# Kernel optimization log

Hardware: AMD Instinct MI355X
Metric: run time of the kernel (lower is better)

## Reference

```python
import jax, jax.numpy as jnp
import numpy as np

D_IN = 2048
D_OUT = 2048
H = 16
QK_ROPE = 64
QK_NOPE = 64
QK_HEAD = QK_NOPE + QK_ROPE  # 128
V_HEAD = 128
KV_RANK = 512
THETA = 10000.0
EPS = 1e-6


def rms_norm(x, w):
    var = jnp.mean(x * x, axis=-1, keepdims=True)
    return x * jax.lax.rsqrt(var + EPS) * w


def apply_rope(x, theta=THETA):
    # x: [B, S, H, D] with D even; interleaved-pair rotation (torchtune style)
    B, S, NH, D = x.shape
    half = D // 2
    freqs = 1.0 / (theta ** (jnp.arange(0, D, 2, dtype=jnp.float32) / D))  # [D/2]
    ang = jnp.arange(S, dtype=jnp.float32)[:, None] * freqs[None, :]       # [S, D/2]
    cos = jnp.cos(ang)[None, :, None, :]  # [1,S,1,D/2]
    sin = jnp.sin(ang)[None, :, None, :]
    xp = x.reshape(B, S, NH, half, 2)
    x1, x2 = xp[..., 0], xp[..., 1]
    out = jnp.stack([x1 * cos - x2 * sin, x2 * cos + x1 * sin], axis=-1)
    return out.reshape(B, S, NH, D).astype(x.dtype)


def setup_inputs() -> dict:
    key = jax.random.key(0)
    ks = jax.random.split(key, 6)
    B, S = 2, 2048
    s = lambda fan_in: 1.0 / np.sqrt(fan_in)
    x = jax.random.normal(ks[0], (B, S, D_IN), dtype=jnp.float32)
    w_query = jax.random.uniform(ks[1], (D_IN, H * QK_HEAD), jnp.float32, -s(D_IN), s(D_IN))
    wkv_a = jax.random.uniform(ks[2], (D_IN, KV_RANK + QK_ROPE), jnp.float32, -s(D_IN), s(D_IN))
    wkv_b = jax.random.uniform(ks[3], (KV_RANK, H * (QK_NOPE + V_HEAD)), jnp.float32, -s(KV_RANK), s(KV_RANK))
    kv_norm_w = jnp.ones((KV_RANK,), jnp.float32)
    out_proj_w = jax.random.uniform(ks[4], (H * V_HEAD, D_OUT), jnp.float32, -s(H * V_HEAD), s(H * V_HEAD))
    return {"x": x, "w_query": w_query, "wkv_a": wkv_a, "wkv_b": wkv_b,
            "kv_norm_w": kv_norm_w, "out_proj_w": out_proj_w}


def reference(x, w_query, wkv_a, wkv_b, kv_norm_w, out_proj_w):
    B, S, _ = x.shape
    scale = QK_HEAD ** -0.5
    # queries (no q-lora)
    q = (x @ w_query).reshape(B, S, H, QK_HEAD)
    # low-rank KV compression
    kv = x @ wkv_a                                    # [B,S,KV_RANK+QK_ROPE]
    kv_c, k_pe = kv[..., :KV_RANK], kv[..., KV_RANK:]
    kv_dec = (rms_norm(kv_c, kv_norm_w) @ wkv_b).reshape(B, S, H, QK_NOPE + V_HEAD)
    k_nope, v = kv_dec[..., :QK_NOPE], kv_dec[..., QK_NOPE:]
    k_pe = jnp.broadcast_to(k_pe[:, :, None, :], (B, S, H, QK_ROPE))
    q_nope, q_pe = q[..., :QK_NOPE], q[..., QK_NOPE:]
    q_pe = apply_rope(q_pe)
    k_pe = apply_rope(k_pe)
    queries = jnp.concatenate([q_nope, q_pe], axis=-1)   # [B,S,H,QK_HEAD]
    keys = jnp.concatenate([k_nope, k_pe], axis=-1)
    # attention
    scores = jnp.einsum('bqhd,bkhd->bhqk', queries, keys) * scale
    mask = jnp.triu(jnp.ones((S, S), dtype=bool), k=1)
    scores = jnp.where(mask[None, None], -jnp.inf, scores)
    attn = jax.nn.softmax(scores.astype(jnp.float32), axis=-1).astype(x.dtype)
    out = jnp.einsum('bhqk,bkhd->bqhd', attn, v).reshape(B, S, H * V_HEAD)
    return out @ out_proj_w
```

## Files before the change

kernel.cpp:

```cpp
#include <hip/hip_runtime.h>
#include <hip/hip_bf16.h>
#include <math.h>

#define BATCH   2
#define SEQ     2048
#define D_IN    2048
#define NHEAD   16
#define QK_ROPE 64
#define QK_NOPE 64
#define QK_HEAD 128
#define V_HEAD  128
#define KV_RANK 512
#define KV_W    640
#define NTOK    (BATCH*SEQ)
#define EPS_F   1e-6f

typedef unsigned short u16;
typedef short bf16x8 __attribute__((ext_vector_type(8)));
typedef float f32x4  __attribute__((ext_vector_type(4)));

__device__ __forceinline__ u16 f2bf(float f) {
    unsigned u = __float_as_uint(f);
    return (u16)((u + 0x7fffu + ((u >> 16) & 1u)) >> 16);
}
__device__ __forceinline__ float bf2f(u16 u) {
    return __uint_as_float(((unsigned)u) << 16);
}
__device__ __forceinline__ float exp2_hw(float x) {
    float r;
    asm volatile("v_exp_f32 %0, %1\n\ts_nop 0" : "=v"(r) : "v"(x));
    return r;
}
__device__ __forceinline__ void gload16(const void* g, void* l) {
    __builtin_amdgcn_global_load_lds((const __attribute__((address_space(1))) unsigned int*)g,
                                     (__attribute__((address_space(3))) unsigned int*)l, 16, 0, 0);
}

__global__ __launch_bounds__(256) void convert_bf16(const float* __restrict__ src,
                                                    u16* __restrict__ dst, int n4) {
    int gid = blockIdx.x * 256 + threadIdx.x;
    if (gid >= n4) return;
    float4 v = ((const float4*)src)[gid];
    unsigned lo = (unsigned)f2bf(v.x) | ((unsigned)f2bf(v.y) << 16);
    unsigned hi = (unsigned)f2bf(v.z) | ((unsigned)f2bf(v.w) << 16);
    ((uint2*)dst)[gid] = make_uint2(lo, hi);
}

__global__ __launch_bounds__(256) void transpose_bf16(const float* __restrict__ src,
                                                      u16* __restrict__ dst,
                                                      int N, int K) {
    __shared__ float tile[32][33];
    const int nb = blockIdx.x * 32, kb = blockIdx.y * 32;
    const int tx = threadIdx.x, ty = threadIdx.y;
#pragma unroll
    for (int i = 0; i < 4; ++i) {
        int k = kb + ty + 8 * i, n = nb + tx;
        tile[ty + 8 * i][tx] = (n < N) ? src[(size_t)k * N + n] : 0.f;
    }
    __syncthreads();
#pragma unroll
    for (int i = 0; i < 4; ++i) {
        int n = nb + ty + 8 * i, k = kb + tx;
        dst[(size_t)n * K + k] = f2bf(tile[tx][ty + 8 * i]);
    }
}

__global__ __launch_bounds__(256) void rope_table_kernel(float* __restrict__ tab) {
    int gid = blockIdx.x * 256 + threadIdx.x;
    int i = gid & 31, s = gid >> 5;
    float freq = __expf(-(float)(2 * i) / 64.0f * 9.210340371976184f);
    float ang = (float)s * freq;
    tab[2 * gid]     = cosf(ang);
    tab[2 * gid + 1] = sinf(ang);
}

template <int EPI>
__global__ __launch_bounds__(256) void gemm_core(const u16* __restrict__ A,
                                                 const u16* __restrict__ BT,
                                                 void* __restrict__ out0,
                                                 void* __restrict__ out1,
                                                 const float* __restrict__ tab,
                                                 int M, int N, int K, float oscale) {
    __shared__ u16 As[128 * 32];
    __shared__ u16 Bs[128 * 32];
    const int tid = threadIdx.x;
    const int w = tid >> 6, l = tid & 63;
    const int lr = l & 15, lg = l >> 4;
    const int wr = w >> 1, wc = w & 1;
    const int row0 = blockIdx.y * 128, col0 = blockIdx.x * 128;

    f32x4 acc[4][4];
#pragma unroll
    for (int a = 0; a < 4; ++a)
#pragma unroll
        for (int b = 0; b < 4; ++b) acc[a][b] = (f32x4){0.f, 0.f, 0.f, 0.f};

    const u16* ga = A + (size_t)(row0 + 32 * w + (l >> 2)) * K + 8 * (l & 3);
    const u16* gb = BT + (size_t)(col0 + 32 * w + (l >> 2)) * K + 8 * (l & 3);
    u16* la = As + w * 1024;
    u16* lb = Bs + w * 1024;

    for (int k0 = 0; k0 < K; k0 += 32) {
        __syncthreads();
        gload16(ga + k0, la);
        gload16(ga + (size_t)16 * K + k0, la + 512);
        gload16(gb + k0, lb);
        gload16(gb + (size_t)16 * K + k0, lb + 512);
        __syncthreads();
        bf16x8 af[4], bfr[4];
#pragma unroll
        for (int mi = 0; mi < 4; ++mi)
            af[mi] = *(const bf16x8*)&As[(64 * wr + 16 * mi + lr) * 32 + 8 * lg];
#pragma unroll
        for (int ni = 0; ni < 4; ++ni)
            bfr[ni] = *(const bf16x8*)&Bs[(64 * wc + 16 * ni + lr) * 32 + 8 * lg];
#pragma unroll
        for (int mi = 0; mi < 4; ++mi)
#pragma unroll
            for (int ni = 0; ni < 4; ++ni)
                acc[mi][ni] = __builtin_amdgcn_mfma_f32_16x16x32_bf16(af[mi], bfr[ni], acc[mi][ni], 0, 0, 0);
    }

    if (EPI == 0) {
        if (col0 < 2048) {
            u16* q = (u16*)out0;
            const bool pe = (wc == 1);
#pragma unroll
            for (int mi = 0; mi < 4; ++mi)
#pragma unroll
                for (int ni = 0; ni < 4; ++ni) {
                    int c = col0 + 64 * wc + 16 * ni + lr;
#pragma unroll
                    for (int j = 0; j < 4; ++j) {
                        int r = row0 + 64 * wr + 16 * mi + 4 * lg + j;
                        float v = acc[mi][ni][j] * oscale;
                        if (pe) {
                            int s = r & (SEQ - 1);
                            int ip = (16 * ni + lr) >> 1;
                            float2 cs = ((const float2*)tab)[s * 32 + ip];
                            float part = __shfl_xor(v, 1);
                            v = (lr & 1) ? (v * cs.x + part * cs.y)
                                         : (v * cs.x - part * cs.y);
                        }
                        q[(size_t)r * 2048 + c] = f2bf(v);
                    }
                }
        } else {
            float* kvp = (float*)out1;
#pragma unroll
            for (int mi = 0; mi < 4; ++mi)
#pragma unroll
                for (int ni = 0; ni < 4; ++ni) {
                    int c = col0 - 2048 + 64 * wc + 16 * ni + lr;
#pragma unroll
                    for (int j = 0; j < 4; ++j) {
                        int r = row0 + 64 * wr + 16 * mi + 4 * lg + j;
                        kvp[(size_t)r * KV_W + c] = acc[mi][ni][j];
                    }
                }
        }
    } else if (EPI == 1) {
        float* C = (float*)out0;
#pragma unroll
        for (int mi = 0; mi < 4; ++mi)
#pragma unroll
            for (int ni = 0; ni < 4; ++ni)
#pragma unroll
                for (int j = 0; j < 4; ++j) {
                    int r = row0 + 64 * wr + 16 * mi + 4 * lg + j;
                    int c = col0 + 64 * wc + 16 * ni + lr;
                    C[(size_t)r * N + c] = acc[mi][ni][j];
                }
    } else {
        u16* Kall = (u16*)out0;
        u16* Vt   = (u16*)out1;
        const int b  = row0 >> 11;
        const int sb = (row0 & (SEQ - 1)) + 64 * wr + 4 * lg;
#pragma unroll
        for (int mi = 0; mi < 4; ++mi) {
            int s0 = sb + 16 * mi;
#pragma unroll
            for (int ni = 0; ni < 4; ++ni) {
                int c = col0 + 64 * wc + 16 * ni + lr;
                int h = (unsigned)c / 192u;
                int cr = c - h * 192;
                int bh = b * NHEAD + h;
                if (cr < 64) {
#pragma unroll
                    for (int j = 0; j < 4; ++j) {
                        int s = s0 + j;
                        Kall[((size_t)bh * SEQ + s) * 128 + (cr ^ ((s & 7) << 3))] = f2bf(acc[mi][ni][j]);
                    }
                } else {
                    int d = cr - 64;
                    union { u16 u[4]; uint2 v; } pk;
#pragma unroll
                    for (int j = 0; j < 4; ++j) pk.u[j] = f2bf(acc[mi][ni][j]);
                    size_t base = ((size_t)bh * 128 + d) * SEQ + (s0 & ~63);
                    *(uint2*)&Vt[base + ((s0 & 63) ^ ((d & 7) << 3))] = pk.v;
                }
            }
        }
    }
}

__global__ __launch_bounds__(256) void rmsnorm_bf(const float* __restrict__ kv,
                                                  const float* __restrict__ w,
                                                  u16* __restrict__ c_norm) {
    __shared__ float red[256];
    const int row = blockIdx.x, t = threadIdx.x;
    const float* src = kv + (size_t)row * KV_W;
    float v0 = src[t], v1 = src[t + 256];
    red[t] = v0 * v0 + v1 * v1;
    __syncthreads();
    for (int s = 128; s > 0; s >>= 1) {
        if (t < s) red[t] += red[t + s];
        __syncthreads();
    }
    const float inv = rsqrtf(red[0] / (float)KV_RANK + EPS_F);
    u16* dst = c_norm + (size_t)row * KV_RANK;
    dst[t]       = f2bf(v0 * inv * w[t]);
    dst[t + 256] = f2bf(v1 * inv * w[t + 256]);
}

__global__ __launch_bounds__(256) void build_kpe(const float* __restrict__ kv,
                                                 const float* __restrict__ tab,
                                                 u16* __restrict__ K_all) {
    const int gid = blockIdx.x * 256 + threadIdx.x;
    const int dq = gid & 15;
    const int s = (gid >> 4) & (SEQ - 1);
    const int b = gid >> 15;
    const float* src = kv + (size_t)(b * SEQ + s) * KV_W + KV_RANK + 4 * dq;
    float4 v = *(const float4*)src;
    const int i0 = 2 * dq;
    float2 cs0 = ((const float2*)tab)[s * 32 + i0];
    float2 cs1 = ((const float2*)tab)[s * 32 + i0 + 1];
    union { u16 u[4]; uint2 w; } pk;
    pk.u[0] = f2bf(v.x * cs0.x - v.y * cs0.y);
    pk.u[1] = f2bf(v.y * cs0.x + v.x * cs0.y);
    pk.u[2] = f2bf(v.z * cs1.x - v.w * cs1.y);
    pk.u[3] = f2bf(v.w * cs1.x + v.z * cs1.y);
    const int idx = (64 + 4 * dq) ^ ((s & 7) << 3);
#pragma unroll
    for (int h = 0; h < NHEAD; ++h) {
        int bh = b * NHEAD + h;
        *(uint2*)&K_all[((size_t)bh * SEQ + s) * 128 + idx] = pk.w;
    }
}

#define QTILE 64
#define KTILE 64

__global__ __launch_bounds__(256, 2) void attn_mfma(const u16* __restrict__ q_bf,
                                                    const u16* __restrict__ K_all,
                                                    const u16* __restrict__ Vt,
                                                    u16* __restrict__ attn_bf) {
    __shared__ u16 Kbuf[2][KTILE * 128];
    __shared__ u16 Vbuf[2][128 * KTILE];
    __shared__ u16 Plds[4][16 * KTILE];

    const int idx = blockIdx.x;
    const int bh = (idx & 7) + 8 * (idx >> 7);
    const int pi = (idx >> 3) & 15;
    const int b = bh >> 4, h = bh & 15;

    const int tid = threadIdx.x;
    const int w = tid >> 6, l = tid & 63;
    const int lr = l & 15, lg = l >> 4;
    const u16* Kb = K_all + (size_t)bh * SEQ * 128;
    const u16* Vb = Vt + (size_t)bh * 128 * SEQ;
    const int sw = (lr & 7) << 3;
    u16* pw = Plds[w];

    auto stage = [&](int bufi, int k0) {
        u16* kb = Kbuf[bufi];
        u16* vb = Vbuf[bufi];
#pragma unroll
        for (int it = 0; it < 4; ++it) {
            int ci = it * 256 + tid;
            gload16(Kb + (((size_t)(k0 + (ci >> 4))) << 7) + ((ci & 15) << 3),
                    kb + (ci << 3));
        }
#pragma unroll
        for (int it = 0; it < 4; ++it) {
            int ci = it * 256 + tid;
            gload16(Vb + (size_t)(ci >> 3) * SEQ + k0 + ((ci & 7) << 3),
                    vb + (ci << 3));
        }
    };

    const int qbA = (31 - pi) * QTILE;
    const int qbB = pi * QTILE;

    stage(0, 0);
    int cur = 0;
    for (int half = 0; half < 2; ++half) {
        const int qbase = half ? qbB : qbA;
        const int nkt = (qbase >> 6) + 1;
        const int qg = qbase + 16 * w + lr;

        const u16* qrow = q_bf + (size_t)(b * SEQ + qg) * 2048 + h * QK_HEAD;
        bf16x8 qf[4];
#pragma unroll
        for (int dc = 0; dc < 4; ++dc) qf[dc] = *(const bf16x8*)(qrow + dc * 32 + lg * 8);

        f32x4 oacc[8];
#pragma unroll
        for (int ft = 0; ft < 8; ++ft) oacc[ft] = (f32x4){0.f, 0.f, 0.f, 0.f};
        float m_r = -1e30f, l_r = 0.f;

        for (int kt = 0; kt < nkt; ++kt) {
            const int k0 = kt * KTILE;
            if (kt + 1 < nkt) {
                stage(cur ^ 1, k0 + KTILE);
                asm volatile("s_waitcnt vmcnt(8)" ::: "memory");
            } else if (half == 0) {
                stage(cur ^ 1, 0);
                asm volatile("s_waitcnt vmcnt(8)" ::: "memory");
            } else {
                asm volatile("s_waitcnt vmcnt(0)" ::: "memory");
            }
            __builtin_amdgcn_s_barrier();
            __builtin_amdgcn_sched_barrier(0);

            const u16* kb = Kbuf[cur];
            const u16* vb = Vbuf[cur];

            f32x4 s[4];
            __builtin_amdgcn_s_setprio(1);
#pragma unroll
            for (int f = 0; f < 4; ++f) {
                s[f] = (f32x4){0.f, 0.f, 0.f, 0.f};
#pragma unroll
                for (int dc = 0; dc < 4; ++dc) {
                    bf16x8 kf = *(const bf16x8*)&kb[(16 * f + lr) * 128 + ((32 * dc + 8 * lg) ^ sw)];
                    s[f] = __builtin_amdgcn_mfma_f32_16x16x32_bf16(kf, qf[dc], s[f], 0, 0, 0);
                }
            }
            __builtin_amdgcn_s_setprio(0);

            if (kt == nkt - 1) {
#pragma unroll
                for (int f = 0; f < 4; ++f)
#pragma unroll
                    for (int j = 0; j < 4; ++j)
                        if (k0 + 16 * f + 4 * lg + j > qg) s[f][j] = -1e30f;
            }

            float t0 = fmaxf(fmaxf(s[0][0], s[0][1]), fmaxf(s[0][2], s[0][3]));
            float t1 = fmaxf(fmaxf(s[1][0], s[1][1]), fmaxf(s[1][2], s[1][3]));
            float t2 = fmaxf(fmaxf(s[2][0], s[2][1]), fmaxf(s[2][2], s[2][3]));
            float t3 = fmaxf(fmaxf(s[3][0], s[3][1]), fmaxf(s[3][2], s[3][3]));
            float t = fmaxf(fmaxf(t0, t1), fmaxf(t2, t3));
            t = fmaxf(t, __shfl_xor(t, 16));
            t = fmaxf(t, __shfl_xor(t, 32));
            bool up = (t > m_r + 11.5f);
            float newm = up ? t : m_r;
            float sf_ = up ? exp2_hw(m_r - t) : 1.0f;
            m_r = newm;
            float rs = 0.f;
#pragma unroll
            for (int f = 0; f < 4; ++f)
#pragma unroll
                for (int j = 0; j < 4; ++j) {
                    float p = exp2_hw(s[f][j] - newm);
                    s[f][j] = p;
                    rs += p;
                }
            rs += __shfl_xor(rs, 16);
            rs += __shfl_xor(rs, 32);
            l_r = l_r * sf_ + rs;
            if (__any(up)) {
#pragma unroll
                for (int ft = 0; ft < 8; ++ft)
#pragma unroll
                    for (int j = 0; j < 4; ++j) oacc[ft][j] *= sf_;
            }

#pragma unroll
            for (int f = 0; f < 4; ++f) {
                union { u16 u[4]; uint2 v; } pk;
#pragma unroll
                for (int j = 0; j < 4; ++j) pk.u[j] = f2bf(s[f][j]);
                *(uint2*)&pw[lr * 64 + ((16 * f + 4 * lg) ^ sw)] = pk.v;
            }
            asm volatile("s_waitcnt lgkmcnt(0)" ::: "memory");
            bf16x8 pfr[2];
#pragma unroll
            for (int ks = 0; ks < 2; ++ks)
                pfr[ks] = *(const bf16x8*)&pw[lr * 64 + ((32 * ks + 8 * lg) ^ sw)];

            __builtin_amdgcn_s_setprio(1);
#pragma unroll
            for (int ft = 0; ft < 8; ++ft) {
                int d = 16 * ft + lr;
#pragma unroll
                for (int ks = 0; ks < 2; ++ks) {
                    bf16x8 vf = *(const bf16x8*)&vb[d * 64 + ((32 * ks + 8 * lg) ^ sw)];
                    oacc[ft] = __builtin_amdgcn_mfma_f32_16x16x32_bf16(vf, pfr[ks], oacc[ft], 0, 0, 0);
                }
            }
            __builtin_amdgcn_s_setprio(0);

            __builtin_amdgcn_s_barrier();
            cur ^= 1;
        }

        const float inv = 1.0f / l_r;
        u16* orow = attn_bf + (size_t)(b * SEQ + qg) * 2048 + h * V_HEAD;
#pragma unroll
        for (int ft = 0; ft < 8; ++ft) {
            union { u16 u[4]; uint2 v; } ok;
#pragma unroll
            for (int j = 0; j < 4; ++j) ok.u[j] = f2bf(oacc[ft][j] * inv);
            *(uint2*)(orow + 16 * ft + 4 * lg) = ok.v;
        }
    }
}

extern "C" void kernel_launch(void* const* d_in, const int* in_sizes, int n_in,
                              void* d_out, int out_size, void* d_ws, size_t ws_size,
                              hipStream_t stream) {
    const float* x         = (const float*)d_in[0];
    const float* w_query   = (const float*)d_in[1];
    const float* wkv_a     = (const float*)d_in[2];
    const float* wkv_b     = (const float*)d_in[3];
    const float* kv_norm_w = (const float*)d_in[4];
    const float* out_proj  = (const float*)d_in[5];

    u16* x_bf     = (u16*)d_ws;
    u16* q_bf     = x_bf + (size_t)8388608;
    u16* c_norm   = q_bf + (size_t)8388608;
    u16* kvdec_bf = c_norm + (size_t)2097152;
    u16* K_all    = kvdec_bf + (size_t)12582912;
    u16* Vt       = K_all + (size_t)8388608;
    u16* wT       = Vt + (size_t)8388608;
    u16* wkvaT    = wT + (size_t)4194304;
    u16* wkvbT    = wkvaT + (size_t)1310720;
    u16* opT      = wkvbT + (size_t)1572864;
    float* kv     = (float*)(opT + (size_t)4194304);
    float* tab    = kv + (size_t)2621440;
    u16* attn_bf  = x_bf;
    float* out = (float*)d_out;

    dim3 tb(32, 8);
    const float qscale2 = 0.08838834764831845f * 1.4426950408889634f;

    convert_bf16<<<8192, 256, 0, stream>>>(x, x_bf, 2097152);
    transpose_bf16<<<dim3(64, 64), tb, 0, stream>>>(w_query, wT, 2048, 2048);
    transpose_bf16<<<dim3(20, 64), tb, 0, stream>>>(wkv_a, wkvaT, 576, 2048);
    transpose_bf16<<<dim3(96, 16), tb, 0, stream>>>(wkv_b, wkvbT, 3072, 512);
    transpose_bf16<<<dim3(64, 64), tb, 0, stream>>>(out_proj, opT, 2048, 2048);
    rope_table_kernel<<<256, 256, 0, stream>>>(tab);

    gemm_core<0><<<dim3(21, 32), 256, 0, stream>>>(x_bf, wT, q_bf, kv, tab,
                                                   NTOK, 2688, 2048, qscale2);
    rmsnorm_bf<<<NTOK, 256, 0, stream>>>(kv, kv_norm_w, c_norm);
    gemm_core<2><<<dim3(24, 32), 256, 0, stream>>>(c_norm, wkvbT, K_all, Vt, nullptr,
                                                   NTOK, 3072, 512, 1.0f);
    build_kpe<<<256, 256, 0, stream>>>(kv, tab, K_all);

    attn_mfma<<<512, 256, 0, stream>>>(q_bf, K_all, Vt, attn_bf);

    gemm_core<1><<<dim3(16, 32), 256, 0, stream>>>(attn_bf, opT, out, nullptr, nullptr,
                                                   NTOK, 2048, 2048, 1.0f);
}
```

Before: 266.8 us.

## Replace 128x128 GEMM with double-buffered swizzled 256x256 tile kernel

Replaces the single-buffered 128x128 GEMM core with a 512-thread kernel that uses 256x256 output tiles and a K-step of 64. Both operands are double-buffered in a 128 KB LDS buffer with an XOR swizzle. Loads for the next K-tile are issued in four stages, one per MFMA sub-block, so global loads overlap compute, and the MFMA section runs at raised wave priority. The goal is more data reuse per block and hiding memory latency. The trade-off is far fewer blocks (128–192 across the three GEMMs), which may leave many CUs idle. The QKV/kv GEMM now also reads past the end of its weight rows in the last column tile, and those results are masked off.

```diff
diff --git a/kernel.cpp b/kernel.cpp
--- a/kernel.cpp
+++ b/kernel.cpp
@@ -75,113 +75,155 @@
 }
 
 template <int EPI>
-__global__ __launch_bounds__(256) void gemm_core(const u16* __restrict__ A,
-                                                 const u16* __restrict__ BT,
-                                                 void* __restrict__ out0,
-                                                 void* __restrict__ out1,
-                                                 const float* __restrict__ tab,
-                                                 int M, int N, int K, float oscale) {
-    __shared__ u16 As[128 * 32];
-    __shared__ u16 Bs[128 * 32];
+__global__ __launch_bounds__(512, 1) void gemm256(const u16* __restrict__ A,
+                                                  const u16* __restrict__ BT,
+                                                  void* __restrict__ out0,
+                                                  void* __restrict__ out1,
+                                                  const float* __restrict__ tab,
+                                                  int N, int K, float oscale) {
+    __shared__ u16 lds[65536];
     const int tid = threadIdx.x;
     const int w = tid >> 6, l = tid & 63;
     const int lr = l & 15, lg = l >> 4;
-    const int wr = w >> 1, wc = w & 1;
-    const int row0 = blockIdx.y * 128, col0 = blockIdx.x * 128;
-
-    f32x4 acc[4][4];
-#pragma unroll
-    for (int a = 0; a < 4; ++a)
-#pragma unroll
-        for (int b = 0; b < 4; ++b) acc[a][b] = (f32x4){0.f, 0.f, 0.f, 0.f};
-
-    const u16* ga = A + (size_t)(row0 + 32 * w + (l >> 2)) * K + 8 * (l & 3);
-    const u16* gb = BT + (size_t)(col0 + 32 * w + (l >> 2)) * K + 8 * (l & 3);
-    u16* la = As + w * 1024;
-    u16* lb = Bs + w * 1024;
-
-    for (int k0 = 0; k0 < K; k0 += 32) {
-        __syncthreads();
-        gload16(ga + k0, la);
-        gload16(ga + (size_t)16 * K + k0, la + 512);
-        gload16(gb + k0, lb);
-        gload16(gb + (size_t)16 * K + k0, lb + 512);
-        __syncthreads();
-        bf16x8 af[4], bfr[4];
-#pragma unroll
-        for (int mi = 0; mi < 4; ++mi)
-            af[mi] = *(const bf16x8*)&As[(64 * wr + 16 * mi + lr) * 32 + 8 * lg];
-#pragma unroll
-        for (int ni = 0; ni < 4; ++ni)
-            bfr[ni] = *(const bf16x8*)&Bs[(64 * wc + 16 * ni + lr) * 32 + 8 * lg];
-#pragma unroll
-        for (int mi = 0; mi < 4; ++mi)
-#pragma unroll
-            for (int ni = 0; ni < 4; ++ni)
-                acc[mi][ni] = __builtin_amdgcn_mfma_f32_16x16x32_bf16(af[mi], bfr[ni], acc[mi][ni], 0, 0, 0);
+    const int wr = w >> 2;
+    const int wc = w & 3;
+    const int row0 = blockIdx.y * 256, col0 = blockIdx.x * 256;
+    const int NT = K >> 6;
+
+    f32x4 acc[8][4];
+#pragma unroll
+    for (int m = 0; m < 8; ++m)
+#pragma unroll
+        for (int n = 0; n < 4; ++n) acc[m][n] = (f32x4){0.f, 0.f, 0.f, 0.f};
+
+    auto stageA = [&](int bufi, int h, int kt) {
+        u16* base = lds + bufi * 16384 + h * 8192;
+        const u16* g = A + (size_t)(row0 + h * 128) * K + kt * 64;
+#pragma unroll
+        for (int i = 0; i < 2; ++i) {
+            int L = (i * 512 + tid) * 16;
+            int s = L ^ (((L >> 7) & 7) << 4);
+            gload16(g + (size_t)(s >> 7) * K + ((s & 127) >> 1), base + (L >> 1));
+        }
+    };
+    auto stageB = [&](int bufi, int h, int kt) {
+        u16* base = lds + 32768 + bufi * 16384 + h * 8192;
+        const u16* g = BT + (size_t)(col0 + h * 128) * K + kt * 64;
+#pragma unroll
+        for (int i = 0; i < 2; ++i) {
+            int L = (i * 512 + tid) * 16;
+            int s = L ^ (((L >> 7) & 7) << 4);
+            gload16(g + (size_t)(s >> 7) * K + ((s & 127) >> 1), base + (L >> 1));
+        }
+    };
+
+    stageA(0, 0, 0); stageA(0, 1, 0); stageB(0, 0, 0); stageB(0, 1, 0);
+
+    const int bhalf = wc >> 1;
+    const int brow0 = (wc & 1) * 64;
+
+    for (int t = 0; t < NT; ++t) {
+        const int buf = t & 1, nb = buf ^ 1;
+        u16* Ab = lds + buf * 16384 + wr * 8192;
+        u16* Bb = lds + 32768 + buf * 16384 + bhalf * 8192;
+        asm volatile("s_waitcnt vmcnt(0)" ::: "memory");
+        __builtin_amdgcn_s_barrier();
+        __builtin_amdgcn_sched_barrier(0);
+
+#pragma unroll
+        for (int q = 0; q < 4; ++q) {
+            bf16x8 af[2][2], bfg[4][2];
+#pragma unroll
+            for (int m2 = 0; m2 < 2; ++m2)
+#pragma unroll
+                for (int ks = 0; ks < 2; ++ks) {
+                    int row = (2 * q + m2) * 16 + lr;
+                    int byte = row * 128 + ks * 64 + lg * 16;
+                    af[m2][ks] = *(const bf16x8*)&Ab[(byte ^ ((row & 7) << 4)) >> 1];
+                }
+#pragma unroll
+            for (int n = 0; n < 4; ++n)
+#pragma unroll
+                for (int ks = 0; ks < 2; ++ks) {
+                    int row = brow0 + n * 16 + lr;
+                    int byte = row * 128 + ks * 64 + lg * 16;
+                    bfg[n][ks] = *(const bf16x8*)&Bb[(byte ^ ((row & 7) << 4)) >> 1];
+                }
+            if (t + 1 < NT) {
+                if (q == 0)      stageA(nb, 0, t + 1);
+                else if (q == 1) stageA(nb, 1, t + 1);
+                else if (q == 2) stageB(nb, 0, t + 1);
+                else             stageB(nb, 1, t + 1);
+            }
+            __builtin_amdgcn_s_barrier();
+            asm volatile("s_waitcnt lgkmcnt(0)" ::: "memory");
+            __builtin_amdgcn_sched_barrier(0);
+            __builtin_amdgcn_s_setprio(1);
+#pragma unroll
+            for (int m2 = 0; m2 < 2; ++m2)
+#pragma unroll
+                for (int n = 0; n < 4; ++n)
+#pragma unroll
+                    for (int ks = 0; ks < 2; ++ks)
+                        acc[2 * q + m2][n] = __builtin_amdgcn_mfma_f32_16x16x32_bf16(
+                            af[m2][ks], bfg[n][ks], acc[2 * q + m2][n], 0, 0, 0);
+            __builtin_amdgcn_s_setprio(0);
+        }
     }
 
     if (EPI == 0) {
-        if (col0 < 2048) {
-            u16* q = (u16*)out0;
-            const bool pe = (wc == 1);
-#pragma unroll
-            for (int mi = 0; mi < 4; ++mi)
-#pragma unroll
-                for (int ni = 0; ni < 4; ++ni) {
-                    int c = col0 + 64 * wc + 16 * ni + lr;
-#pragma unroll
-                    for (int j = 0; j < 4; ++j) {
-                        int r = row0 + 64 * wr + 16 * mi + 4 * lg + j;
-                        float v = acc[mi][ni][j] * oscale;
+        u16* qp = (u16*)out0;
+        float* kvp = (float*)out1;
+        const bool pe = (wc & 1);
+#pragma unroll
+        for (int m = 0; m < 8; ++m)
+#pragma unroll
+            for (int n = 0; n < 4; ++n) {
+                int c = col0 + wc * 64 + n * 16 + lr;
+#pragma unroll
+                for (int j = 0; j < 4; ++j) {
+                    int r = row0 + wr * 128 + m * 16 + 4 * lg + j;
+                    float v = acc[m][n][j];
+                    if (c < 2048) {
+                        v *= oscale;
                         if (pe) {
                             int s = r & (SEQ - 1);
-                            int ip = (16 * ni + lr) >> 1;
+                            int ip = (16 * n + lr) >> 1;
                             float2 cs = ((const float2*)tab)[s * 32 + ip];
                             float part = __shfl_xor(v, 1);
                             v = (lr & 1) ? (v * cs.x + part * cs.y)
                                          : (v * cs.x - part * cs.y);
                         }
-                        q[(size_t)r * 2048 + c] = f2bf(v);
+                        qp[(size_t)r * 2048 + c] = f2bf(v);
+                    } else if (c < 2688) {
+                        kvp[(size_t)r * KV_W + (c - 2048)] = v;
                     }
                 }
-        } else {
-            float* kvp = (float*)out1;
-#pragma unroll
-            for (int mi = 0; mi < 4; ++mi)
-#pragma unroll
-                for (int ni = 0; ni < 4; ++ni) {
-                    int c = col0 - 2048 + 64 * wc + 16 * ni + lr;
-#pragma unroll
-                    for (int j = 0; j < 4; ++j) {
-                        int r = row0 + 64 * wr + 16 * mi + 4 * lg + j;
-                        kvp[(size_t)r * KV_W + c] = acc[mi][ni][j];
-                    }
-                }
-        }
+            }
     } else if (EPI == 1) {
         float* C = (float*)out0;
 #pragma unroll
-        for (int mi = 0; mi < 4; ++mi)
-#pragma unroll
-            for (int ni = 0; ni < 4; ++ni)
+        for (int m = 0; m < 8; ++m)
+#pragma unroll
+            for (int n = 0; n < 4; ++n) {
+                int c = col0 + wc * 64 + n * 16 + lr;
 #pragma unroll
                 for (int j = 0; j < 4; ++j) {
-                    int r = row0 + 64 * wr + 16 * mi + 4 * lg + j;
-                    int c = col0 + 64 * wc + 16 * ni + lr;
-                    C[(size_t)r * N + c] = acc[mi][ni][j];
-                }
+                    int r = row0 + wr * 128 + m * 16 + 4 * lg + j;
+                    C[(size_t)r * N + c] = acc[m][n][j];
+                }
+            }
     } else {
         u16* Kall = (u16*)out0;
         u16* Vt   = (u16*)out1;
-        const int b  = row0 >> 11;
-        const int sb = (row0 & (SEQ - 1)) + 64 * wr + 4 * lg;
-#pragma unroll
-        for (int mi = 0; mi < 4; ++mi) {
-            int s0 = sb + 16 * mi;
-#pragma unroll
-            for (int ni = 0; ni < 4; ++ni) {
-                int c = col0 + 64 * wc + 16 * ni + lr;
+#pragma unroll
+        for (int m = 0; m < 8; ++m) {
+            int r0 = row0 + wr * 128 + m * 16 + 4 * lg;
+            int b  = r0 >> 11;
+            int s0 = r0 & (SEQ - 1);
+#pragma unroll
+            for (int n = 0; n < 4; ++n) {
+                int c = col0 + wc * 64 + n * 16 + lr;
                 int h = (unsigned)c / 192u;
                 int cr = c - h * 192;
                 int bh = b * NHEAD + h;
@@ -189,13 +231,13 @@
 #pragma unroll
                     for (int j = 0; j < 4; ++j) {
                         int s = s0 + j;
-                        Kall[((size_t)bh * SEQ + s) * 128 + (cr ^ ((s & 7) << 3))] = f2bf(acc[mi][ni][j]);
+                        Kall[((size_t)bh * SEQ + s) * 128 + (cr ^ ((s & 7) << 3))] = f2bf(acc[m][n][j]);
                     }
                 } else {
                     int d = cr - 64;
                     union { u16 u[4]; uint2 v; } pk;
 #pragma unroll
-                    for (int j = 0; j < 4; ++j) pk.u[j] = f2bf(acc[mi][ni][j]);
+                    for (int j = 0; j < 4; ++j) pk.u[j] = f2bf(acc[m][n][j]);
                     size_t base = ((size_t)bh * 128 + d) * SEQ + (s0 & ~63);
                     *(uint2*)&Vt[base + ((s0 & 63) ^ ((d & 7) << 3))] = pk.v;
                 }
@@ -453,15 +495,15 @@
     transpose_bf16<<<dim3(64, 64), tb, 0, stream>>>(out_proj, opT, 2048, 2048);
     rope_table_kernel<<<256, 256, 0, stream>>>(tab);
 
-    gemm_core<0><<<dim3(21, 32), 256, 0, stream>>>(x_bf, wT, q_bf, kv, tab,
-                                                   NTOK, 2688, 2048, qscale2);
+    gemm256<0><<<dim3(11, 16), 512, 0, stream>>>(x_bf, wT, q_bf, kv, tab,
+                                                 2688, 2048, qscale2);
     rmsnorm_bf<<<NTOK, 256, 0, stream>>>(kv, kv_norm_w, c_norm);
-    gemm_core<2><<<dim3(24, 32), 256, 0, stream>>>(c_norm, wkvbT, K_all, Vt, nullptr,
-                                                   NTOK, 3072, 512, 1.0f);
+    gemm256<2><<<dim3(12, 16), 512, 0, stream>>>(c_norm, wkvbT, K_all, Vt, nullptr,
+                                                 3072, 512, 1.0f);
     build_kpe<<<256, 256, 0, stream>>>(kv, tab, K_all);
 
     attn_mfma<<<512, 256, 0, stream>>>(q_bf, K_all, Vt, attn_bf);
 
-    gemm_core<1><<<dim3(16, 32), 256, 0, stream>>>(attn_bf, opT, out, nullptr, nullptr,
-                                                   NTOK, 2048, 2048, 1.0f);
-}
+    gemm256<1><<<dim3(8, 16), 512, 0, stream>>>(attn_bf, opT, out, nullptr, nullptr,
+                                                2048, 2048, 1.0f);
+}
```

Result: slower. 277.7 us (+4.1%).
